# Optimization experiments

Measured on AMD Instinct MI355X. Metric: run time of the kernel, lower is better.

The kernel has to match this reference:

```python
import jax, jax.numpy as jnp
import numpy as np

N_NODES = 50000
N_EDGES = 800000
IN_DIM = 64
HID = 128
OUT_DIM = 64
T_HIST = 8


def setup_inputs() -> dict:
    key = jax.random.key(0)
    ks = jax.random.split(key, 12)
    s = 0.05
    return {
        "node_feats": jax.random.normal(ks[0], (N_NODES, IN_DIM), jnp.float32),
        "history_feats": jax.random.normal(ks[1], (N_NODES, T_HIST, HID), jnp.float32),
        "src": jax.random.randint(ks[2], (N_EDGES,), 0, N_NODES, jnp.int32),
        "dst": jax.random.randint(ks[3], (N_EDGES,), 0, N_NODES, jnp.int32),
        # SAGEConv params (fc_self, fc_neigh share bias as in DGL)
        "W_self": jax.random.normal(ks[4], (IN_DIM, HID), jnp.float32) * s,
        "W_neigh": jax.random.normal(ks[5], (IN_DIM, HID), jnp.float32) * s,
        "b_sage": jnp.zeros((HID,), jnp.float32),
        # LSTM params, PyTorch gate order [i, f, g, o]
        "w_ih": jax.random.normal(ks[6], (HID, 4 * HID), jnp.float32) * s,
        "w_hh": jax.random.normal(ks[7], (HID, 4 * HID), jnp.float32) * s,
        "b_lstm": jnp.zeros((4 * HID,), jnp.float32),
        # classifier
        "W_cls": jax.random.normal(ks[8], (HID, OUT_DIM), jnp.float32) * s,
        "b_cls": jnp.zeros((OUT_DIM,), jnp.float32),
    }


def _lstm_last(x, w_ih, w_hh, b):
    # x: [N, T, H] -> last hidden state [N, H]
    N, T, H = x.shape

    def step(carry, xt):
        h, c = carry
        gates = xt @ w_ih + h @ w_hh + b  # [N, 4H]
        i, f, g, o = jnp.split(gates, 4, axis=-1)
        c = jax.nn.sigmoid(f) * c + jax.nn.sigmoid(i) * jnp.tanh(g)
        h = jax.nn.sigmoid(o) * jnp.tanh(c)
        return (h, c), None

    h0 = jnp.zeros((N, H), x.dtype)
    (h, _), _ = jax.lax.scan(step, (h0, h0), jnp.swapaxes(x, 0, 1))
    return h


def reference(node_feats, history_feats, src, dst, W_self, W_neigh, b_sage,
              w_ih, w_hh, b_lstm, W_cls, b_cls):
    N = node_feats.shape[0]
    # SAGEConv mean aggregation: mean of in-neighbor features per dst node
    msg_sum = jax.ops.segment_sum(node_feats[src], dst, num_segments=N)
    deg = jax.ops.segment_sum(jnp.ones((src.shape[0],), node_feats.dtype),
                              dst, num_segments=N)
    h_neigh = msg_sum / jnp.maximum(deg, 1.0)[:, None]
    h_struct = node_feats @ W_self + h_neigh @ W_neigh + b_sage  # [N, HID]
    # LSTM over history, take last timestep
    h_temp = _lstm_last(history_feats, w_ih, w_hh, b_lstm)  # [N, HID]
    h_combined = h_struct + h_temp
    return h_combined @ W_cls + b_cls  # [N, OUT_DIM]
```

## Files before the change

kernel.cpp:

```cpp
#include <hip/hip_runtime.h>
#include <hip/hip_bf16.h>
#include <stdint.h>

#define N_NODES 50000
#define N_EDGES 800000
#define IN_DIM 64
#define HID 128
#define OUT_DIM 64
#define T_HIST 8

#define NB_SCAN ((N_NODES + 1023) / 1024)

typedef __attribute__((ext_vector_type(8))) short short8;
typedef __attribute__((ext_vector_type(4))) float f32x4;

__device__ __forceinline__ unsigned short f2bf(float x) {
  unsigned int u = __builtin_bit_cast(unsigned int, x);
  unsigned int r = (u + 0x7FFFu + ((u >> 16) & 1u)) >> 16;
  return (unsigned short)r;
}
__device__ __forceinline__ short8 cvt8(float4 a, float4 b) {
  unsigned int w0, w1, w2, w3;
  asm("v_cvt_pk_bf16_f32 %0, %1, %2" : "=v"(w0) : "v"(a.x), "v"(a.y));
  asm("v_cvt_pk_bf16_f32 %0, %1, %2" : "=v"(w1) : "v"(a.z), "v"(a.w));
  asm("v_cvt_pk_bf16_f32 %0, %1, %2" : "=v"(w2) : "v"(b.x), "v"(b.y));
  asm("v_cvt_pk_bf16_f32 %0, %1, %2" : "=v"(w3) : "v"(b.z), "v"(b.w));
  struct { unsigned int a, b, c, d; } s{w0, w1, w2, w3};
  return __builtin_bit_cast(short8, s);
}
__device__ __forceinline__ float sigm(float x) {
  float e = __builtin_amdgcn_exp2f(-1.4426950408889634f * x);
  return __builtin_amdgcn_rcpf(1.f + e);
}
__device__ __forceinline__ float tanh_f(float x) {
  float e = __builtin_amdgcn_exp2f(2.8853900817779268f * x);
  return 1.f - 2.f * __builtin_amdgcn_rcpf(e + 1.f);
}

__global__ void pc_kernel(const float* __restrict__ w_ih, const float* __restrict__ w_hh,
                          const float* __restrict__ W_cls,
                          const float* __restrict__ W_self, const float* __restrict__ W_neigh,
                          const float* __restrict__ b_sage, const float* __restrict__ b_cls,
                          const int* __restrict__ dst,
                          unsigned short* __restrict__ Wt2, unsigned short* __restrict__ Wc2,
                          float* __restrict__ Wsc, float* __restrict__ Wnc,
                          float* __restrict__ bc1, int* __restrict__ cnt) {
  int tid = blockIdx.x * blockDim.x + threadIdx.x;
  int stride = gridDim.x * blockDim.x;
  for (int e = tid; e < N_EDGES; e += stride) atomicAdd(&cnt[dst[e]], 1);
  for (int idx = tid; idx < 256 * 512; idx += stride) {
    int i = idx & 7;
    int lane = (idx >> 3) & 63;
    int F = idx >> 9;
    int q = F >> 5, g = (F >> 3) & 3, kk = F & 7;
    int c = g * 128 + q * 16 + (lane & 15);
    int k = kk * 32 + (lane >> 4) * 8 + i;
    float v = (k < 128) ? w_ih[k * 512 + c] : w_hh[(k - 128) * 512 + c];
    Wt2[idx] = f2bf(v);
  }
  for (int idx = tid; idx < 16 * 512; idx += stride) {
    int i = idx & 7;
    int lane = (idx >> 3) & 63;
    int F = idx >> 9;
    int cb = F >> 2, kk = F & 3;
    int col = cb * 16 + (lane & 15);
    int k = kk * 32 + (lane >> 4) * 8 + i;
    Wc2[idx] = f2bf(W_cls[k * 64 + col]);
  }
  for (int idx = tid; idx < 64 * 64; idx += stride) {
    int k = idx >> 6, c = idx & 63;
    float as = 0.f, an = 0.f;
    for (int m = 0; m < 128; m++) {
      float wc = W_cls[m * 64 + c];
      as += W_self[k * 128 + m] * wc;
      an += W_neigh[k * 128 + m] * wc;
    }
    Wsc[idx] = as;
    Wnc[idx] = an;
  }
  for (int c = tid; c < 64; c += stride) {
    float acc = b_cls[c];
    for (int m = 0; m < 128; m++) acc += b_sage[m] * W_cls[m * 64 + c];
    bc1[c] = acc;
  }
}

__global__ __launch_bounds__(256) void scan1_kernel(const int* __restrict__ cnt,
                                                    int* __restrict__ lexcl, int* __restrict__ btot) {
  __shared__ int sh[256];
  int tid = threadIdx.x;
  int base = blockIdx.x * 1024 + tid * 4;
  int v[4];
  #pragma unroll
  for (int q = 0; q < 4; q++) {
    int i = base + q;
    v[q] = (i < N_NODES) ? cnt[i] : 0;
  }
  int tsum = v[0] + v[1] + v[2] + v[3];
  sh[tid] = tsum;
  __syncthreads();
  int val = tsum;
  for (int off = 1; off < 256; off <<= 1) {
    int x = (tid >= off) ? sh[tid - off] : 0;
    __syncthreads();
    val += x;
    sh[tid] = val;
    __syncthreads();
  }
  int ex = val - tsum;
  if (tid == 255) btot[blockIdx.x] = val;
  #pragma unroll
  for (int q = 0; q < 4; q++) {
    int i = base + q;
    if (i < N_NODES) lexcl[i] = ex;
    ex += v[q];
  }
}

__global__ __launch_bounds__(1024) void scan3_kernel(const int* __restrict__ lexcl,
                                                     const int* __restrict__ btot,
                                                     int* __restrict__ rowstart, int* __restrict__ cursor) {
  int b = blockIdx.x;
  int bs = 0;
  for (int j = 0; j < b; j++) bs += btot[j];
  int i = b * 1024 + threadIdx.x;
  if (i < N_NODES) {
    int rs = lexcl[i] + bs;
    rowstart[i] = rs;
    cursor[i] = rs;
  }
}

__global__ void fill_kernel(const int* __restrict__ src, const int* __restrict__ dst,
                            int* __restrict__ cursor, int* __restrict__ esrc) {
  int e = blockIdx.x * blockDim.x + threadIdx.x;
  if (e < N_EDGES) {
    int d = dst[e];
    int pos = atomicAdd(&cursor[d], 1);
    esrc[pos] = src[e];
  }
}

#define HS_TILE 32
__global__ __launch_bounds__(512) void hstruct_kernel(
    const float* __restrict__ nf, const int* __restrict__ esrc,
    const int* __restrict__ rowstart, const int* __restrict__ cnt,
    const float* __restrict__ Wsc, const float* __restrict__ Wnc, const float* __restrict__ bc1,
    float* __restrict__ out1) {
  __shared__ float s_nf[HS_TILE][IN_DIM + 1];
  __shared__ float s_hn[HS_TILE][IN_DIM + 1];
  int tid = threadIdx.x;
  int node0 = blockIdx.x * HS_TILE;
  for (int i = tid; i < HS_TILE * IN_DIM; i += 512) {
    int r = i >> 6, k = i & 63;
    int node = node0 + r;
    s_nf[r][k] = (node < N_NODES) ? nf[node * 64 + k] : 0.f;
  }
  int wv = tid >> 6, lane = tid & 63;
  for (int r = wv; r < HS_TILE; r += 8) {
    int node = node0 + r;
    float a0 = 0.f, a1 = 0.f, a2 = 0.f, a3 = 0.f;
    int n = 0;
    if (node < N_NODES) {
      n = cnt[node];
      int st = rowstart[node];
      int j = 0;
      for (; j + 4 <= n; j += 4) {
        int s0 = esrc[st + j], s1 = esrc[st + j + 1];
        int s2 = esrc[st + j + 2], s3 = esrc[st + j + 3];
        a0 += nf[s0 * 64 + lane];
        a1 += nf[s1 * 64 + lane];
        a2 += nf[s2 * 64 + lane];
        a3 += nf[s3 * 64 + lane];
      }
      for (; j < n; j++) a0 += nf[esrc[st + j] * 64 + lane];
    }
    s_hn[r][lane] = (a0 + a1 + a2 + a3) * __builtin_amdgcn_rcpf(fmaxf((float)n, 1.f));
  }
  __syncthreads();
  int r = tid & 31;
  int c0 = (tid >> 5) * 4;
  float accs[4] = {0.f, 0.f, 0.f, 0.f};
  for (int k = 0; k < IN_DIM; k++) {
    float a = s_nf[r][k];
    float b = s_hn[r][k];
    float4 w1 = *(const float4*)&Wsc[k * 64 + c0];
    float4 w2 = *(const float4*)&Wnc[k * 64 + c0];
    accs[0] += a * w1.x + b * w2.x;
    accs[1] += a * w1.y + b * w2.y;
    accs[2] += a * w1.z + b * w2.z;
    accs[3] += a * w1.w + b * w2.w;
  }
  int node = node0 + r;
  if (node < N_NODES) {
    #pragma unroll
    for (int i = 0; i < 4; i++)
      out1[(size_t)node * 64 + c0 + i] = accs[i] + bc1[c0 + i];
  }
}

#define LB 32
__global__ __launch_bounds__(512, 2) void lstm_kernel(
    const float* __restrict__ hist,
    const unsigned short* __restrict__ Wt2,
    const unsigned short* __restrict__ Wc2,
    const float* __restrict__ b_lstm,
    const float* __restrict__ out1,
    float* __restrict__ out)
{
  __shared__ alignas(16) unsigned short Abuf[2][LB * 256];

  const int tid = threadIdx.x;
  const int lane = tid & 63;
  const int w = tid >> 6;
  const int l15 = lane & 15;
  const int l4 = lane >> 4;
  const int base = blockIdx.x * LB;
  const int jj = w * 16 + l15;

  short8 Bfr[4][8];
  #pragma unroll
  for (int g = 0; g < 4; g++)
    #pragma unroll
    for (int kk = 0; kk < 8; kk++)
      Bfr[g][kk] = *(const short8*)&Wt2[((w * 32 + g * 8 + kk) * 64 + lane) * 8];

  const float bi  = b_lstm[jj];
  const float bf_ = b_lstm[128 + jj];
  const float bg  = b_lstm[256 + jj];
  const float bo  = b_lstm[384 + jj];

  float c_st[8];
  #pragma unroll
  for (int i = 0; i < 8; i++) c_st[i] = 0.f;

  {
    int row = tid >> 4;
    int kb = tid & 15;
    short8 z = {0,0,0,0,0,0,0,0};
    *(short8*)&Abuf[0][row * 256 + 128 + kb * 8] = z;
    int node = base + row;
    float4 x0 = make_float4(0.f,0.f,0.f,0.f), x1 = make_float4(0.f,0.f,0.f,0.f);
    if (node < N_NODES) {
      const float4* p = (const float4*)&hist[(size_t)node * (T_HIST * HID) + kb * 8];
      x0 = p[0]; x1 = p[1];
    }
    int sb = (kb & 8) | ((kb & 7) ^ (row & 7));
    *(short8*)&Abuf[0][row * 256 + sb * 8] = cvt8(x0, x1);
  }
  __syncthreads();

  float4 xpa, xpb;
  const int srow = tid >> 4, skb = tid & 15;

  #pragma unroll
  for (int t = 0; t < T_HIST - 1; t++) {
    unsigned short* Acur = &Abuf[t & 1][0];
    unsigned short* Anxt = &Abuf[(t & 1) ^ 1][0];

    {
      int node = base + srow;
      if (node < N_NODES) {
        const float4* p = (const float4*)&hist[(size_t)node * (T_HIST * HID) + (t + 1) * HID + skb * 8];
        xpa = p[0]; xpb = p[1];
      } else {
        xpa = make_float4(0.f,0.f,0.f,0.f);
        xpb = make_float4(0.f,0.f,0.f,0.f);
      }
    }

    #pragma unroll
    for (int rb = 0; rb < 2; rb++) {
      f32x4 acc[4];
      #pragma unroll
      for (int g = 0; g < 4; g++) { f32x4 z = {0.f,0.f,0.f,0.f}; acc[g] = z; }
      #pragma unroll
      for (int kk = 0; kk < 8; kk++) {
        int row = rb * 16 + l15;
        int kb = kk * 4 + l4;
        int sb = (kb & 24) | ((kb & 7) ^ (row & 7));
        short8 a = *(const short8*)&Acur[row * 256 + sb * 8];
        #pragma unroll
        for (int g = 0; g < 4; g++)
          acc[g] = __builtin_amdgcn_mfma_f32_16x16x32_bf16(a, Bfr[g][kk], acc[g], 0, 0, 0);
      }
      #pragma unroll
      for (int reg = 0; reg < 4; reg++) {
        int r = rb * 4 + reg;
        float gi = sigm(acc[0][reg] + bi);
        float gf = sigm(acc[1][reg] + bf_);
        float gg = tanh_f(acc[2][reg] + bg);
        float go = sigm(acc[3][reg] + bo);
        float c = gf * c_st[r] + gi * gg;
        c_st[r] = c;
        float h = go * tanh_f(c);
        int row = rb * 16 + l4 * 4 + reg;
        int kb = 16 + (jj >> 3);
        int sb = (kb & 24) | ((kb & 7) ^ (row & 7));
        Anxt[row * 256 + sb * 8 + (jj & 7)] = f2bf(h);
      }
    }

    {
      int sb = (skb & 8) | ((skb & 7) ^ (srow & 7));
      *(short8*)&Anxt[srow * 256 + sb * 8] = cvt8(xpa, xpb);
    }
    __syncthreads();
  }

  {
    unsigned short* Acur = &Abuf[1][0];
    unsigned short* Anxt = &Abuf[0][0];

    #pragma unroll
    for (int rb = 0; rb < 2; rb++) {
      f32x4 acc[4];
      #pragma unroll
      for (int g = 0; g < 4; g++) { f32x4 z = {0.f,0.f,0.f,0.f}; acc[g] = z; }
      #pragma unroll
      for (int kk = 0; kk < 8; kk++) {
        int row = rb * 16 + l15;
        int kb = kk * 4 + l4;
        int sb = (kb & 24) | ((kb & 7) ^ (row & 7));
        short8 a = *(const short8*)&Acur[row * 256 + sb * 8];
        #pragma unroll
        for (int g = 0; g < 4; g++)
          acc[g] = __builtin_amdgcn_mfma_f32_16x16x32_bf16(a, Bfr[g][kk], acc[g], 0, 0, 0);
      }
      #pragma unroll
      for (int reg = 0; reg < 4; reg++) {
        int r = rb * 4 + reg;
        float gi = sigm(acc[0][reg] + bi);
        float gf = sigm(acc[1][reg] + bf_);
        float gg = tanh_f(acc[2][reg] + bg);
        float go = sigm(acc[3][reg] + bo);
        float c = gf * c_st[r] + gi * gg;
        float h = go * tanh_f(c);
        int row = rb * 16 + l4 * 4 + reg;
        int kb = jj >> 3;
        int sb = (kb & 8) | ((kb & 7) ^ (row & 7));
        Anxt[row * 256 + sb * 8 + (jj & 7)] = f2bf(h);
      }
    }
    __syncthreads();

    {
      int rbo = w >> 2, cbo = w & 3;
      int col = cbo * 16 + l15;
      float ov[4];
      #pragma unroll
      for (int reg = 0; reg < 4; reg++) {
        int row = rbo * 16 + l4 * 4 + reg;
        int node = base + row;
        ov[reg] = (node < N_NODES) ? out1[(size_t)node * OUT_DIM + col] : 0.f;
      }
      f32x4 o = {0.f, 0.f, 0.f, 0.f};
      #pragma unroll
      for (int kk = 0; kk < 4; kk++) {
        short8 bv = *(const short8*)&Wc2[((cbo * 4 + kk) * 64 + lane) * 8];
        int row = rbo * 16 + l15;
        int kb = kk * 4 + l4;
        int sb = (kb & 8) | ((kb & 7) ^ (row & 7));
        short8 a = *(const short8*)&Anxt[row * 256 + sb * 8];
        o = __builtin_amdgcn_mfma_f32_16x16x32_bf16(a, bv, o, 0, 0, 0);
      }
      #pragma unroll
      for (int reg = 0; reg < 4; reg++) {
        int row = rbo * 16 + l4 * 4 + reg;
        int node = base + row;
        if (node < N_NODES) out[(size_t)node * OUT_DIM + col] = o[reg] + ov[reg];
      }
    }
  }
}

extern "C" void kernel_launch(void* const* d_in, const int* in_sizes, int n_in,
                              void* d_out, int out_size, void* d_ws, size_t ws_size,
                              hipStream_t stream) {
  (void)in_sizes; (void)n_in; (void)out_size; (void)ws_size;
  const float* node_feats = (const float*)d_in[0];
  const float* hist       = (const float*)d_in[1];
  const int*   src        = (const int*)d_in[2];
  const int*   dst        = (const int*)d_in[3];
  const float* W_self     = (const float*)d_in[4];
  const float* W_neigh    = (const float*)d_in[5];
  const float* b_sage     = (const float*)d_in[6];
  const float* w_ih       = (const float*)d_in[7];
  const float* w_hh       = (const float*)d_in[8];
  const float* b_lstm     = (const float*)d_in[9];
  const float* W_cls      = (const float*)d_in[10];
  const float* b_cls      = (const float*)d_in[11];
  float* out = (float*)d_out;

  char* ws = (char*)d_ws;
  int* cnt        = (int*)(ws);
  int* lexcl      = (int*)(ws + 200192);
  int* rowstart   = (int*)(ws + 400384);
  int* cursor     = (int*)(ws + 600576);
  int* btot       = (int*)(ws + 800768);
  int* esrc       = (int*)(ws + 801792);
  float* out1     = (float*)(ws + 4001792);
  unsigned short* Wt2 = (unsigned short*)(ws + 16801792);
  unsigned short* Wc2 = (unsigned short*)(ws + 17063936);
  float* Wsc      = (float*)(ws + 17080320);
  float* Wnc      = (float*)(ws + 17096704);
  float* bc1      = (float*)(ws + 17113088);

  hipMemsetAsync(cnt, 0, 200000, stream);
  pc_kernel<<<1024, 256, 0, stream>>>(w_ih, w_hh, W_cls, W_self, W_neigh, b_sage, b_cls,
                                      dst, Wt2, Wc2, Wsc, Wnc, bc1, cnt);
  scan1_kernel<<<NB_SCAN, 256, 0, stream>>>(cnt, lexcl, btot);
  scan3_kernel<<<NB_SCAN, 1024, 0, stream>>>(lexcl, btot, rowstart, cursor);
  fill_kernel<<<(N_EDGES + 255) / 256, 256, 0, stream>>>(src, dst, cursor, esrc);
  hstruct_kernel<<<(N_NODES + HS_TILE - 1) / HS_TILE, 512, 0, stream>>>(
      node_feats, esrc, rowstart, cnt, Wsc, Wnc, bc1, out1);
  lstm_kernel<<<(N_NODES + LB - 1) / LB, 512, 0, stream>>>(
      hist, Wt2, Wc2, b_lstm, out1, out);
}
```

Measured before the change: 357.8 us.

## Fuse CSR build kernels into one persistent kernel with grid barriers

```diff
diff --git a/kernel.cpp b/kernel.cpp
--- a/kernel.cpp
+++ b/kernel.cpp
@@ -9,7 +9,8 @@
 #define OUT_DIM 64
 #define T_HIST 8
 
-#define NB_SCAN ((N_NODES + 1023) / 1024)
+#define CSR_NB 49
+#define CSR_NT 1024
 
 typedef __attribute__((ext_vector_type(8))) short short8;
 typedef __attribute__((ext_vector_type(4))) float f32x4;
@@ -37,18 +38,36 @@
   return 1.f - 2.f * __builtin_amdgcn_rcpf(e + 1.f);
 }
 
-__global__ void pc_kernel(const float* __restrict__ w_ih, const float* __restrict__ w_hh,
-                          const float* __restrict__ W_cls,
-                          const float* __restrict__ W_self, const float* __restrict__ W_neigh,
-                          const float* __restrict__ b_sage, const float* __restrict__ b_cls,
-                          const int* __restrict__ dst,
-                          unsigned short* __restrict__ Wt2, unsigned short* __restrict__ Wc2,
-                          float* __restrict__ Wsc, float* __restrict__ Wnc,
-                          float* __restrict__ bc1, int* __restrict__ cnt) {
-  int tid = blockIdx.x * blockDim.x + threadIdx.x;
-  int stride = gridDim.x * blockDim.x;
-  for (int e = tid; e < N_EDGES; e += stride) atomicAdd(&cnt[dst[e]], 1);
-  for (int idx = tid; idx < 256 * 512; idx += stride) {
+__device__ __forceinline__ void gbar(int* bar, int target) {
+  __syncthreads();
+  __threadfence();
+  if (threadIdx.x == 0) {
+    atomicAdd(bar, 1);
+    while (atomicAdd(bar, 0) < target) __builtin_amdgcn_s_sleep(8);
+  }
+  __syncthreads();
+}
+
+__global__ __launch_bounds__(CSR_NT) void csr_kernel(
+    const int* __restrict__ src, const int* __restrict__ dst,
+    const float* __restrict__ w_ih, const float* __restrict__ w_hh,
+    const float* __restrict__ W_cls, const float* __restrict__ W_self,
+    const float* __restrict__ W_neigh, const float* __restrict__ b_sage,
+    const float* __restrict__ b_cls,
+    unsigned short* __restrict__ Wt2, unsigned short* __restrict__ Wc2,
+    float* __restrict__ Wsc, float* __restrict__ Wnc, float* __restrict__ bc1,
+    int* __restrict__ cnt, int* __restrict__ rowstart, int* __restrict__ cursor,
+    int* __restrict__ btot, int* __restrict__ esrc, int* __restrict__ bar)
+{
+  __shared__ int sh[CSR_NT];
+  __shared__ int s_bs;
+  const int tid = threadIdx.x;
+  const int b = blockIdx.x;
+  const int gtid = b * CSR_NT + tid;
+  const int GS = CSR_NB * CSR_NT;
+
+  for (int i = gtid; i < N_NODES; i += GS) atomicExch(&cnt[i], 0);
+  for (int idx = gtid; idx < 256 * 512; idx += GS) {
     int i = idx & 7;
     int lane = (idx >> 3) & 63;
     int F = idx >> 9;
@@ -58,7 +77,7 @@
     float v = (k < 128) ? w_ih[k * 512 + c] : w_hh[(k - 128) * 512 + c];
     Wt2[idx] = f2bf(v);
   }
-  for (int idx = tid; idx < 16 * 512; idx += stride) {
+  for (int idx = gtid; idx < 16 * 512; idx += GS) {
     int i = idx & 7;
     int lane = (idx >> 3) & 63;
     int F = idx >> 9;
@@ -67,7 +86,7 @@
     int k = kk * 32 + (lane >> 4) * 8 + i;
     Wc2[idx] = f2bf(W_cls[k * 64 + col]);
   }
-  for (int idx = tid; idx < 64 * 64; idx += stride) {
+  for (int idx = gtid; idx < 64 * 64; idx += GS) {
     int k = idx >> 6, c = idx & 63;
     float as = 0.f, an = 0.f;
     for (int m = 0; m < 128; m++) {
@@ -78,63 +97,48 @@
     Wsc[idx] = as;
     Wnc[idx] = an;
   }
-  for (int c = tid; c < 64; c += stride) {
+  for (int c = gtid; c < 64; c += GS) {
     float acc = b_cls[c];
     for (int m = 0; m < 128; m++) acc += b_sage[m] * W_cls[m * 64 + c];
     bc1[c] = acc;
   }
-}
-
-__global__ __launch_bounds__(256) void scan1_kernel(const int* __restrict__ cnt,
-                                                    int* __restrict__ lexcl, int* __restrict__ btot) {
-  __shared__ int sh[256];
-  int tid = threadIdx.x;
-  int base = blockIdx.x * 1024 + tid * 4;
-  int v[4];
-  #pragma unroll
-  for (int q = 0; q < 4; q++) {
-    int i = base + q;
-    v[q] = (i < N_NODES) ? cnt[i] : 0;
-  }
-  int tsum = v[0] + v[1] + v[2] + v[3];
-  sh[tid] = tsum;
-  __syncthreads();
-  int val = tsum;
-  for (int off = 1; off < 256; off <<= 1) {
+  gbar(bar, CSR_NB * 1);
+
+  for (int e = gtid; e < N_EDGES; e += GS) atomicAdd(&cnt[dst[e]], 1);
+  gbar(bar, CSR_NB * 2);
+
+  const int i = b * CSR_NT + tid;
+  int v = (i < N_NODES) ? atomicAdd(&cnt[i], 0) : 0;
+  sh[tid] = v;
+  __syncthreads();
+  int val = v;
+  for (int off = 1; off < CSR_NT; off <<= 1) {
     int x = (tid >= off) ? sh[tid - off] : 0;
     __syncthreads();
     val += x;
     sh[tid] = val;
     __syncthreads();
   }
-  int ex = val - tsum;
-  if (tid == 255) btot[blockIdx.x] = val;
-  #pragma unroll
-  for (int q = 0; q < 4; q++) {
-    int i = base + q;
-    if (i < N_NODES) lexcl[i] = ex;
-    ex += v[q];
-  }
-}
-
-__global__ __launch_bounds__(1024) void scan3_kernel(const int* __restrict__ lexcl,
-                                                     const int* __restrict__ btot,
-                                                     int* __restrict__ rowstart, int* __restrict__ cursor) {
-  int b = blockIdx.x;
-  int bs = 0;
-  for (int j = 0; j < b; j++) bs += btot[j];
-  int i = b * 1024 + threadIdx.x;
+  const int lex = val - v;
+  if (tid == CSR_NT - 1) atomicExch(&btot[b], val);
+  gbar(bar, CSR_NB * 3);
+
+  sh[tid] = (tid < b) ? atomicAdd(&btot[tid], 0) : 0;
+  __syncthreads();
+  if (tid == 0) {
+    int bs = 0;
+    for (int j = 0; j < CSR_NB; j++) bs += sh[j];
+    s_bs = bs;
+  }
+  __syncthreads();
   if (i < N_NODES) {
-    int rs = lexcl[i] + bs;
+    int rs = lex + s_bs;
     rowstart[i] = rs;
-    cursor[i] = rs;
-  }
-}
-
-__global__ void fill_kernel(const int* __restrict__ src, const int* __restrict__ dst,
-                            int* __restrict__ cursor, int* __restrict__ esrc) {
-  int e = blockIdx.x * blockDim.x + threadIdx.x;
-  if (e < N_EDGES) {
+    atomicExch(&cursor[i], rs);
+  }
+  gbar(bar, CSR_NB * 4);
+
+  for (int e = gtid; e < N_EDGES; e += GS) {
     int d = dst[e];
     int pos = atomicAdd(&cursor[d], 1);
     esrc[pos] = src[e];
@@ -394,24 +398,22 @@
 
   char* ws = (char*)d_ws;
   int* cnt        = (int*)(ws);
-  int* lexcl      = (int*)(ws + 200192);
-  int* rowstart   = (int*)(ws + 400384);
-  int* cursor     = (int*)(ws + 600576);
-  int* btot       = (int*)(ws + 800768);
-  int* esrc       = (int*)(ws + 801792);
-  float* out1     = (float*)(ws + 4001792);
-  unsigned short* Wt2 = (unsigned short*)(ws + 16801792);
-  unsigned short* Wc2 = (unsigned short*)(ws + 17063936);
-  float* Wsc      = (float*)(ws + 17080320);
-  float* Wnc      = (float*)(ws + 17096704);
-  float* bc1      = (float*)(ws + 17113088);
-
-  hipMemsetAsync(cnt, 0, 200000, stream);
-  pc_kernel<<<1024, 256, 0, stream>>>(w_ih, w_hh, W_cls, W_self, W_neigh, b_sage, b_cls,
-                                      dst, Wt2, Wc2, Wsc, Wnc, bc1, cnt);
-  scan1_kernel<<<NB_SCAN, 256, 0, stream>>>(cnt, lexcl, btot);
-  scan3_kernel<<<NB_SCAN, 1024, 0, stream>>>(lexcl, btot, rowstart, cursor);
-  fill_kernel<<<(N_EDGES + 255) / 256, 256, 0, stream>>>(src, dst, cursor, esrc);
+  int* rowstart   = (int*)(ws + 200192);
+  int* cursor     = (int*)(ws + 400384);
+  int* btot       = (int*)(ws + 600576);
+  int* bar        = (int*)(ws + 600832);
+  int* esrc       = (int*)(ws + 601088);
+  float* out1     = (float*)(ws + 3801088);
+  unsigned short* Wt2 = (unsigned short*)(ws + 16601088);
+  unsigned short* Wc2 = (unsigned short*)(ws + 16863232);
+  float* Wsc      = (float*)(ws + 16879616);
+  float* Wnc      = (float*)(ws + 16896000);
+  float* bc1      = (float*)(ws + 16912384);
+
+  hipMemsetAsync(bar, 0, 4, stream);
+  csr_kernel<<<CSR_NB, CSR_NT, 0, stream>>>(
+      src, dst, w_ih, w_hh, W_cls, W_self, W_neigh, b_sage, b_cls,
+      Wt2, Wc2, Wsc, Wnc, bc1, cnt, rowstart, cursor, btot, esrc, bar);
   hstruct_kernel<<<(N_NODES + HS_TILE - 1) / HS_TILE, 512, 0, stream>>>(
       node_feats, esrc, rowstart, cnt, Wsc, Wnc, bc1, out1);
   lstm_kernel<<<(N_NODES + LB - 1) / LB, 512, 0, stream>>>(
```

After: 412.9 us. +15.4%, slower.
